# Optimization experiments

Hardware: AMD Instinct MI355X
Metric: run time of the kernel (lower is better)

The kernel has to match this reference:

```python
import jax, jax.numpy as jnp
import numpy as np
import math

N_HEAD = 16
DEG = 2
EPS = 1e-7


def setup_inputs() -> dict:
    key = jax.random.key(0)
    k1, k2 = jax.random.split(key)
    B, T, C = 2, 2048, 1024
    x = jax.random.normal(k1, (B, T, C), dtype=jnp.float32)
    W = jax.random.normal(k2, (3 * C + N_HEAD, C), dtype=jnp.float32) * (1.0 / math.sqrt(C))
    return {"x": x, "W": W}


def reference(x, W):
    # JacobAttentionLayer.forward with attention_kernel='powerref' (AttentionReference,
    # deg=2, scale=1/sqrt(hs), eps=1e-7, log-space power softmax, gating=True).
    B, T, C = x.shape
    nh = N_HEAD
    hs = C // nh
    scale = 1.0 / math.sqrt(hs)

    qkvgr = jnp.einsum('btc,oc->bto', x, W)  # [B,T,3C+nh]
    q, k, v = (qkvgr[..., :C], qkvgr[..., C:2 * C], qkvgr[..., 2 * C:3 * C])
    log_g = jax.nn.log_sigmoid(qkvgr[..., 3 * C:].astype(jnp.float32))  # [B,T,nh]
    log_G = jnp.cumsum(log_g, axis=1).transpose(0, 2, 1)  # [B,nh,T]

    def heads(a):  # [B,T,C] -> [B,nh,T,hs]
        return a.reshape(B, T, nh, hs).transpose(0, 2, 1, 3)

    Q, K, V = heads(q), heads(k), heads(v)

    S = jnp.einsum('bhtd,bhsd->bhts', Q, K)  # [B,nh,T,T]
    # log-space power attention: deg*log(|S|+eps) + log(scale) + gating
    Tm = DEG * jnp.log(jnp.abs(S) + EPS) + jnp.log(jnp.float32(scale))
    Z = Tm + log_G[..., :, None] - log_G[..., None, :]
    mask = jnp.tril(jnp.ones((T, T), dtype=bool))
    Z = jnp.where(mask, Z, -jnp.inf)
    Z_rowmax = jax.lax.stop_gradient(jnp.max(Z, axis=-1, keepdims=True))
    P = jnp.exp(Z - Z_rowmax)  # deg even -> no sign correction

    norm = jnp.sum(P, axis=-1)  # [B,nh,T]
    O = jnp.einsum('bhts,bhsd->bhtd', P, V)
    y = O / norm[..., None]
    return y.transpose(0, 2, 1, 3).reshape(B, T, C)
```

## Files before the change

### kernel.cpp

```cpp
#include <hip/hip_runtime.h>
#include <math.h>

typedef __attribute__((ext_vector_type(4))) float f32x4;
typedef __attribute__((ext_vector_type(8))) short short8;

__device__ __forceinline__ unsigned short f2bf(float f) {
    union { float f; unsigned u; } v; v.f = f;
    unsigned r = v.u + 0x7FFFu + ((v.u >> 16) & 1u);
    return (unsigned short)(r >> 16);
}
__device__ __forceinline__ unsigned short f2bf_trunc(float f) {
    union { float f; unsigned u; } v; v.f = f;
    return (unsigned short)(v.u >> 16);
}
__device__ __forceinline__ float bf2f(unsigned short h) {
    union { unsigned u; float f; } v; v.u = ((unsigned)h) << 16;
    return v.f;
}

__device__ __forceinline__ f32x4 mfma_bf16(short8 a, short8 b, f32x4 c) {
    return __builtin_amdgcn_mfma_f32_16x16x32_bf16(a, b, c, 0, 0, 0);
}

__device__ __forceinline__ void gload_lds16(const unsigned short* g, unsigned short* l) {
    __builtin_amdgcn_global_load_lds(
        (const __attribute__((address_space(1))) void*)g,
        (__attribute__((address_space(3))) void*)l, 16, 0, 0);
}

__global__ void split_all(const float* __restrict__ x,
                          unsigned short* __restrict__ xh, unsigned short* __restrict__ xl,
                          const float* __restrict__ Wm,
                          unsigned short* __restrict__ wh, unsigned short* __restrict__ wl,
                          int nx4, int nw4)
{
    int i = blockIdx.x * 256 + threadIdx.x;
    const float* src; unsigned short* dh; unsigned short* dl; int j;
    if (i < nx4) { src = x; dh = xh; dl = xl; j = i; }
    else if (i < nx4 + nw4) { src = Wm; dh = wh; dl = wl; j = i - nx4; }
    else return;
    float4 v = ((const float4*)src)[j];
    ushort4 h, l;
    h.x = f2bf(v.x); l.x = f2bf(v.x - bf2f(h.x));
    h.y = f2bf(v.y); l.y = f2bf(v.y - bf2f(h.y));
    h.z = f2bf(v.z); l.z = f2bf(v.z - bf2f(h.z));
    h.w = f2bf(v.w); l.w = f2bf(v.w - bf2f(h.w));
    ((ushort4*)dh)[j] = h;
    ((ushort4*)dl)[j] = l;
}

__global__ __launch_bounds__(256, 2)
void gemm_proj(const unsigned short* __restrict__ xh, const unsigned short* __restrict__ xl,
               const unsigned short* __restrict__ wh, const unsigned short* __restrict__ wl,
               unsigned short* __restrict__ Qh, unsigned short* __restrict__ Ql,
               unsigned short* __restrict__ Kh, unsigned short* __restrict__ Kl,
               unsigned short* __restrict__ Vtg, float* __restrict__ gbuf)
{
    __shared__ __align__(16) unsigned short Ah[2][128][32];
    __shared__ __align__(16) unsigned short Al[2][128][32];
    __shared__ __align__(16) unsigned short Bh[2][128][32];
    __shared__ __align__(16) unsigned short Bl[2][128][32];

    const int mt = blockIdx.x & 31;
    const int nt = blockIdx.x >> 5;
    const int m0 = mt * 128, n0 = nt * 128;
    const int tid = threadIdx.x;
    const int w = tid >> 6, l = tid & 63;
    const int wm = w >> 1, wn = w & 1;
    const int lr = l & 15, lq = l >> 4;
    const int xs = (lr >> 1) & 3;
    const bool needLo = (nt < 16) || (nt == 24);

    f32x4 acc[4][4];
#pragma unroll
    for (int i = 0; i < 4; ++i)
#pragma unroll
        for (int j = 0; j < 4; ++j) acc[i][j] = (f32x4){0.f, 0.f, 0.f, 0.f};

    const int srow = tid >> 2;
    const int sp = tid & 3;

    auto STAGE = [&](int bsel, int k0) {
#pragma unroll
        for (int p = 0; p < 2; ++p) {
            int r = srow + p * 64;
            int sc = (sp ^ ((r >> 1) & 3)) * 8;
            int o = n0 + r;
            int oc = o < 3088 ? o : 3087;
            gload_lds16(&xh[(size_t)(m0 + r) * 1024 + k0 + sc], &Ah[bsel][r][sp * 8]);
            gload_lds16(&wh[(size_t)oc * 1024 + k0 + sc],       &Bh[bsel][r][sp * 8]);
            if (needLo) {
                gload_lds16(&xl[(size_t)(m0 + r) * 1024 + k0 + sc], &Al[bsel][r][sp * 8]);
                gload_lds16(&wl[(size_t)oc * 1024 + k0 + sc],       &Bl[bsel][r][sp * 8]);
            }
        }
    };

    STAGE(0, 0);
    __asm__ volatile("s_waitcnt vmcnt(0)" ::: "memory");
    __syncthreads();

    int cur = 0;
    for (int k0 = 0; k0 < 1024; k0 += 32) {
        if (k0 + 32 < 1024) STAGE(cur ^ 1, k0 + 32);

        short8 ah[4], bh4[4], al4[4], bl4[4];
#pragma unroll
        for (int i = 0; i < 4; ++i) {
            ah[i]  = *(const short8*)&Ah[cur][wm * 64 + i * 16 + lr][(lq ^ xs) * 8];
            bh4[i] = *(const short8*)&Bh[cur][wn * 64 + i * 16 + lr][(lq ^ xs) * 8];
        }
        if (needLo) {
#pragma unroll
            for (int i = 0; i < 4; ++i) {
                al4[i] = *(const short8*)&Al[cur][wm * 64 + i * 16 + lr][(lq ^ xs) * 8];
                bl4[i] = *(const short8*)&Bl[cur][wn * 64 + i * 16 + lr][(lq ^ xs) * 8];
            }
        }
#pragma unroll
        for (int i = 0; i < 4; ++i)
#pragma unroll
            for (int j = 0; j < 4; ++j) {
                acc[i][j] = mfma_bf16(ah[i], bh4[j], acc[i][j]);
                if (needLo) {
                    acc[i][j] = mfma_bf16(ah[i], bl4[j], acc[i][j]);
                    acc[i][j] = mfma_bf16(al4[i], bh4[j], acc[i][j]);
                }
            }

        __asm__ volatile("s_waitcnt vmcnt(0)" ::: "memory");
        __syncthreads();
        cur ^= 1;
    }

#pragma unroll
    for (int i = 0; i < 4; ++i) {
        int nrow0 = m0 + wm * 64 + i * 16 + lq * 4;
        int b = nrow0 >> 11;
        int tbase = nrow0 & 2047;
#pragma unroll
        for (int j = 0; j < 4; ++j) {
            int o = n0 + wn * 64 + j * 16 + lr;
            if (o < 1024) {
                int h = o >> 6, d = o & 63;
                size_t base = ((size_t)(b * 16 + h) * 2048 + tbase) * 64 + d;
#pragma unroll
                for (int r = 0; r < 4; ++r) {
                    float v = acc[i][j][r];
                    unsigned short hi_ = f2bf(v);
                    unsigned short lo_ = f2bf(v - bf2f(hi_));
                    Qh[base + (size_t)r * 64] = hi_;
                    Ql[base + (size_t)r * 64] = lo_;
                }
            } else if (o < 2048) {
                int oo = o - 1024;
                int h = oo >> 6, d = oo & 63;
                size_t base = ((size_t)(b * 16 + h) * 2048 + tbase) * 64 + d;
#pragma unroll
                for (int r = 0; r < 4; ++r) {
                    float v = acc[i][j][r];
                    unsigned short hi_ = f2bf(v);
                    unsigned short lo_ = f2bf(v - bf2f(hi_));
                    Kh[base + (size_t)r * 64] = hi_;
                    Kl[base + (size_t)r * 64] = lo_;
                }
            } else if (o < 3072) {
                int oo = o - 2048;
                int h = oo >> 6, d = oo & 63;
                size_t base = ((size_t)(b * 16 + h) * 64 + d) * 2048 + tbase;
                ushort4 pk;
                pk.x = f2bf(acc[i][j][0]);
                pk.y = f2bf(acc[i][j][1]);
                pk.z = f2bf(acc[i][j][2]);
                pk.w = f2bf(acc[i][j][3]);
                *(ushort4*)&Vtg[base] = pk;
            } else if (o < 3088) {
                int og = o - 3072;
#pragma unroll
                for (int r = 0; r < 4; ++r)
                    gbuf[(size_t)(nrow0 + r) * 16 + og] = acc[i][j][r];
            }
        }
    }
}

__global__ void gate_scan(const float* __restrict__ g, float* __restrict__ lg)
{
    const int bh = blockIdx.x;
    const int b = bh >> 4, h = bh & 15;
    const int tid = threadIdx.x;
    __shared__ float part[256];

    float vals[8];
    float run = 0.f;
#pragma unroll
    for (int j = 0; j < 8; ++j) {
        int t = tid * 8 + j;
        float x = g[(size_t)(b * 2048 + t) * 16 + h];
        float ls = fminf(x, 0.f) - log1pf(__expf(-fabsf(x)));
        run += ls * 1.4426950408889634f;
        vals[j] = run;
    }
    part[tid] = run;
    __syncthreads();
    for (int ofs = 1; ofs < 256; ofs <<= 1) {
        float add = (tid >= ofs) ? part[tid - ofs] : 0.f;
        __syncthreads();
        part[tid] += add;
        __syncthreads();
    }
    float excl = part[tid] - run;
#pragma unroll
    for (int j = 0; j < 8; ++j)
        lg[(size_t)bh * 2048 + tid * 8 + j] = excl + vals[j];
}

__global__ __launch_bounds__(256, 3)
void attn_fwd(const unsigned short* __restrict__ Qh, const unsigned short* __restrict__ Ql,
              const unsigned short* __restrict__ Kh, const unsigned short* __restrict__ Kl,
              const unsigned short* __restrict__ Vtg, const float* __restrict__ lg,
              float* __restrict__ out)
{
    __shared__ __align__(16) unsigned short kh[2][64][64];
    __shared__ __align__(16) unsigned short kl[2][64][64];
    __shared__ __align__(16) unsigned short pl[4][16][64];

    const int bid = blockIdx.x;
    const int x8 = bid & 7;
    const int k  = bid >> 3;
    const int bh = x8 + 8 * (k & 3);
    const int m  = k >> 2;
    const int qi = 31 - m;
    const int tid = threadIdx.x;
    const int w = tid >> 6, l = tid & 63;
    const int lr = l & 15, lq = l >> 4;
    const int xk = lr & 7;
    const int q0 = qi * 64;
    const int myrow0 = q0 + w * 16;

    const size_t qoff = ((size_t)bh * 2048 + myrow0 + lr) * 64;
    short8 qh8[2], ql8[2];
    qh8[0] = *(const short8*)&Qh[qoff + lq * 8];
    qh8[1] = *(const short8*)&Qh[qoff + 32 + lq * 8];
    ql8[0] = *(const short8*)&Ql[qoff + lq * 8];
    ql8[1] = *(const short8*)&Ql[qoff + 32 + lq * 8];

    float gq2[4];
#pragma unroll
    for (int r = 0; r < 4; ++r)
        gq2[r] = lg[(size_t)bh * 2048 + myrow0 + lq * 4 + r] - 3.0f;

    f32x4 ls4 = (f32x4){0.f, 0.f, 0.f, 0.f};
    f32x4 o4[4];
#pragma unroll
    for (int i = 0; i < 4; ++i) o4[i] = (f32x4){0.f, 0.f, 0.f, 0.f};

    short8 ones8;
#pragma unroll
    for (int j = 0; j < 8; ++j) ones8[j] = (short)0x3F80;

    const int srow = tid >> 3;
    const int schunk = tid & 7;

    const unsigned short* Kh_b = Kh + (size_t)bh * 2048 * 64;
    const unsigned short* Kl_b = Kl + (size_t)bh * 2048 * 64;
    const unsigned short* Vt_b = Vtg + (size_t)bh * 64 * 2048;

    auto STAGE = [&](int bsel, int kv0) {
#pragma unroll
        for (int p = 0; p < 2; ++p) {
            int r = srow + p * 32;
            int sc = (schunk ^ (r & 7)) * 8;
            gload_lds16(&Kh_b[(size_t)(kv0 + r) * 64 + sc], &kh[bsel][r][schunk * 8]);
            gload_lds16(&Kl_b[(size_t)(kv0 + r) * 64 + sc], &kl[bsel][r][schunk * 8]);
        }
    };

    STAGE(0, 0);
    __asm__ volatile("s_waitcnt vmcnt(0)" ::: "memory");
    __syncthreads();

    int cur = 0;
    for (int kv0 = 0; kv0 <= q0; kv0 += 64) {
        uint4 vreg[8];
#pragma unroll
        for (int ds_ = 0; ds_ < 4; ++ds_) {
            const unsigned short* vp = &Vt_b[(size_t)(ds_ * 16 + lr) * 2048 + kv0 + lq * 8];
            vreg[ds_ * 2]     = *(const uint4*)vp;
            vreg[ds_ * 2 + 1] = *(const uint4*)(vp + 32);
        }
        if (kv0 + 64 <= q0) STAGE(cur ^ 1, kv0 + 64);

        float gsl[4];
#pragma unroll
        for (int js = 0; js < 4; ++js)
            gsl[js] = lg[(size_t)bh * 2048 + kv0 + js * 16 + lr];

        f32x4 sa[4];
#pragma unroll
        for (int js = 0; js < 4; ++js) sa[js] = (f32x4){0.f, 0.f, 0.f, 0.f};
#pragma unroll
        for (int js = 0; js < 4; ++js)
#pragma unroll
            for (int ks = 0; ks < 2; ++ks) {
                short8 kb  = *(const short8*)&kh[cur][js * 16 + lr][((ks * 4 + lq) ^ xk) << 3];
                short8 kbl = *(const short8*)&kl[cur][js * 16 + lr][((ks * 4 + lq) ^ xk) << 3];
                sa[js] = mfma_bf16(qh8[ks], kb,  sa[js]);
                sa[js] = mfma_bf16(qh8[ks], kbl, sa[js]);
                sa[js] = mfma_bf16(ql8[ks], kb,  sa[js]);
            }

        const bool diag = (kv0 == q0);
#pragma unroll
        for (int js = 0; js < 4; ++js) {
            float ga = gsl[js];
#pragma unroll
            for (int r = 0; r < 4; ++r) {
                float a = fabsf(sa[js][r]) + 1e-7f;
                float ex = exp2f(gq2[r] - ga);
                float wv = a * a * ex;
                if (diag && (js * 16 + lr > w * 16 + lq * 4 + r)) wv = 0.f;
                sa[js][r] = wv;
            }
        }

#pragma unroll
        for (int js = 0; js < 4; ++js)
#pragma unroll
            for (int r = 0; r < 4; ++r) {
                int prow = lq * 4 + r;
                int cch = (js * 2 + (lr >> 3)) ^ (prow & 7);
                pl[w][prow][(cch << 3) | (lr & 7)] = f2bf_trunc(sa[js][r]);
            }
        __asm__ volatile("s_waitcnt lgkmcnt(0)" ::: "memory");
        __builtin_amdgcn_sched_barrier(0);

        short8 pa0 = *(const short8*)&pl[w][lr][((0 + lq) ^ xk) << 3];
        short8 pa1 = *(const short8*)&pl[w][lr][((4 + lq) ^ xk) << 3];

        ls4 = mfma_bf16(pa0, ones8, ls4);
        ls4 = mfma_bf16(pa1, ones8, ls4);
#pragma unroll
        for (int ds_ = 0; ds_ < 4; ++ds_) {
            short8 vb0 = *(const short8*)&vreg[ds_ * 2];
            short8 vb1 = *(const short8*)&vreg[ds_ * 2 + 1];
            o4[ds_] = mfma_bf16(pa0, vb0, o4[ds_]);
            o4[ds_] = mfma_bf16(pa1, vb1, o4[ds_]);
        }

        __asm__ volatile("s_waitcnt vmcnt(0)" ::: "memory");
        __syncthreads();
        cur ^= 1;
    }

    const int b = bh >> 4, h = bh & 15;
#pragma unroll
    for (int ds_ = 0; ds_ < 4; ++ds_)
#pragma unroll
        for (int r = 0; r < 4; ++r) {
            int t = myrow0 + lq * 4 + r;
            out[(size_t)(b * 2048 + t) * 1024 + h * 64 + ds_ * 16 + lr] =
                o4[ds_][r] / ls4[r];
        }
}

extern "C" void kernel_launch(void* const* d_in, const int* in_sizes, int n_in,
                              void* d_out, int out_size, void* d_ws, size_t ws_size,
                              hipStream_t stream)
{
    const float* x = (const float*)d_in[0];
    const float* W = (const float*)d_in[1];
    float* out = (float*)d_out;

    const size_t NX = 4194304;
    const size_t NW = 3162112;
    const size_t NQ = 4194304;

    char* ws = (char*)d_ws;
    size_t off = 0;
    auto alloc = [&](size_t bytes) -> void* {
        void* p = ws + off;
        off += (bytes + 255) & ~(size_t)255;
        return p;
    };
    unsigned short* xh = (unsigned short*)alloc(NX * 2);
    unsigned short* xl = (unsigned short*)alloc(NX * 2);
    unsigned short* wh = (unsigned short*)alloc(NW * 2);
    unsigned short* wl = (unsigned short*)alloc(NW * 2);
    unsigned short* Qh = (unsigned short*)alloc(NQ * 2);
    unsigned short* Ql = (unsigned short*)alloc(NQ * 2);
    unsigned short* Kh = (unsigned short*)alloc(NQ * 2);
    unsigned short* Kl = (unsigned short*)alloc(NQ * 2);
    unsigned short* Vt = (unsigned short*)alloc(NQ * 2);
    float* g  = (float*)alloc(65536 * 4);
    float* lg = (float*)alloc(65536 * 4);
    if (off > ws_size) return;

    const int nx4 = (int)(NX / 4), nw4 = (int)(NW / 4);
    split_all<<<(nx4 + nw4 + 255) / 256, 256, 0, stream>>>(x, xh, xl, W, wh, wl, nx4, nw4);
    gemm_proj<<<800, 256, 0, stream>>>(xh, xl, wh, wl, Qh, Ql, Kh, Kl, Vt, g);
    gate_scan<<<32, 256, 0, stream>>>(g, lg);
    attn_fwd<<<1024, 256, 0, stream>>>(Qh, Ql, Kh, Kl, Vt, lg, out);
}
```

Baseline: 183.7 us.

## Drop LDS staging in projection GEMM, load MFMA operands directly from global

The projection GEMM no longer double-buffers A/B tiles through shared memory. Each wave now reads its bf16 hi/lo operand fragments straight from global memory (relying on L1/L2 for reuse), which removes the barriers and LDS traffic. Launch bounds are raised to 3 blocks per SM to gain occupancy. The cost is that operands shared across waves are fetched redundantly from cache and there is no explicit prefetch overlap, so load latency may become exposed.

```diff
diff --git a/kernel.cpp b/kernel.cpp
--- a/kernel.cpp
+++ b/kernel.cpp
@@ -49,18 +49,13 @@
     ((ushort4*)dl)[j] = l;
 }
 
-__global__ __launch_bounds__(256, 2)
+__global__ __launch_bounds__(256, 3)
 void gemm_proj(const unsigned short* __restrict__ xh, const unsigned short* __restrict__ xl,
                const unsigned short* __restrict__ wh, const unsigned short* __restrict__ wl,
                unsigned short* __restrict__ Qh, unsigned short* __restrict__ Ql,
                unsigned short* __restrict__ Kh, unsigned short* __restrict__ Kl,
                unsigned short* __restrict__ Vtg, float* __restrict__ gbuf)
 {
-    __shared__ __align__(16) unsigned short Ah[2][128][32];
-    __shared__ __align__(16) unsigned short Al[2][128][32];
-    __shared__ __align__(16) unsigned short Bh[2][128][32];
-    __shared__ __align__(16) unsigned short Bl[2][128][32];
-
     const int mt = blockIdx.x & 31;
     const int nt = blockIdx.x >> 5;
     const int m0 = mt * 128, n0 = nt * 128;
@@ -68,7 +63,6 @@
     const int w = tid >> 6, l = tid & 63;
     const int wm = w >> 1, wn = w & 1;
     const int lr = l & 15, lq = l >> 4;
-    const int xs = (lr >> 1) & 3;
     const bool needLo = (nt < 16) || (nt == 24);
 
     f32x4 acc[4][4];
@@ -77,45 +71,34 @@
 #pragma unroll
         for (int j = 0; j < 4; ++j) acc[i][j] = (f32x4){0.f, 0.f, 0.f, 0.f};
 
-    const int srow = tid >> 2;
-    const int sp = tid & 3;
-
-    auto STAGE = [&](int bsel, int k0) {
-#pragma unroll
-        for (int p = 0; p < 2; ++p) {
-            int r = srow + p * 64;
-            int sc = (sp ^ ((r >> 1) & 3)) * 8;
-            int o = n0 + r;
-            int oc = o < 3088 ? o : 3087;
-            gload_lds16(&xh[(size_t)(m0 + r) * 1024 + k0 + sc], &Ah[bsel][r][sp * 8]);
-            gload_lds16(&wh[(size_t)oc * 1024 + k0 + sc],       &Bh[bsel][r][sp * 8]);
-            if (needLo) {
-                gload_lds16(&xl[(size_t)(m0 + r) * 1024 + k0 + sc], &Al[bsel][r][sp * 8]);
-                gload_lds16(&wl[(size_t)oc * 1024 + k0 + sc],       &Bl[bsel][r][sp * 8]);
-            }
-        }
-    };
-
-    STAGE(0, 0);
-    __asm__ volatile("s_waitcnt vmcnt(0)" ::: "memory");
-    __syncthreads();
-
-    int cur = 0;
+    const size_t aoff = (size_t)(m0 + wm * 64 + lr) * 1024 + lq * 8;
+    const unsigned short* xA  = xh + aoff;
+    const unsigned short* xAl = xl + aoff;
+    const unsigned short* wB[4];
+    const unsigned short* wBl[4];
+#pragma unroll
+    for (int j = 0; j < 4; ++j) {
+        int o = n0 + wn * 64 + j * 16 + lr;
+        int oc = o < 3088 ? o : 3087;
+        wB[j]  = wh + (size_t)oc * 1024 + lq * 8;
+        wBl[j] = wl + (size_t)oc * 1024 + lq * 8;
+    }
+
     for (int k0 = 0; k0 < 1024; k0 += 32) {
-        if (k0 + 32 < 1024) STAGE(cur ^ 1, k0 + 32);
-
         short8 ah[4], bh4[4], al4[4], bl4[4];
 #pragma unroll
-        for (int i = 0; i < 4; ++i) {
-            ah[i]  = *(const short8*)&Ah[cur][wm * 64 + i * 16 + lr][(lq ^ xs) * 8];
-            bh4[i] = *(const short8*)&Bh[cur][wn * 64 + i * 16 + lr][(lq ^ xs) * 8];
-        }
+        for (int i = 0; i < 4; ++i)
+            ah[i]  = *(const short8*)(xA + (size_t)i * 16 * 1024 + k0);
+#pragma unroll
+        for (int j = 0; j < 4; ++j)
+            bh4[j] = *(const short8*)(wB[j] + k0);
         if (needLo) {
 #pragma unroll
-            for (int i = 0; i < 4; ++i) {
-                al4[i] = *(const short8*)&Al[cur][wm * 64 + i * 16 + lr][(lq ^ xs) * 8];
-                bl4[i] = *(const short8*)&Bl[cur][wn * 64 + i * 16 + lr][(lq ^ xs) * 8];
-            }
+            for (int i = 0; i < 4; ++i)
+                al4[i] = *(const short8*)(xAl + (size_t)i * 16 * 1024 + k0);
+#pragma unroll
+            for (int j = 0; j < 4; ++j)
+                bl4[j] = *(const short8*)(wBl[j] + k0);
         }
 #pragma unroll
         for (int i = 0; i < 4; ++i)
@@ -127,10 +110,6 @@
                     acc[i][j] = mfma_bf16(al4[i], bh4[j], acc[i][j]);
                 }
             }
-
-        __asm__ volatile("s_waitcnt vmcnt(0)" ::: "memory");
-        __syncthreads();
-        cur ^= 1;
     }
 
 #pragma unroll
```

Measured after the change: 287.4 us. 1.56x slower.

## Single-buffer lo-part tiles in projection GEMM and raise occupancy to three blocks

Applied to the files above, without the earlier changes.

The projection GEMM now keeps the bf16 low-part A/B tiles in a single buffer that is loaded inside the current k-step instead of double-buffering them. The hi-part MFMAs run first while the lo loads are in flight, followed by a partial vmcnt wait and a barrier. The freed LDS and a launch-bounds change target three resident blocks per CU. Block order is also remapped so the heavier tile column (nt=24, which needs the lo correction) is scheduled first. In exchange, the lo loads are less hidden, each step gets an extra barrier, and the tighter register budget could cause spills.

```diff
diff --git a/kernel.cpp b/kernel.cpp
--- a/kernel.cpp
+++ b/kernel.cpp
@@ -49,7 +49,7 @@
     ((ushort4*)dl)[j] = l;
 }
 
-__global__ __launch_bounds__(256, 2)
+__global__ __launch_bounds__(256, 3)
 void gemm_proj(const unsigned short* __restrict__ xh, const unsigned short* __restrict__ xl,
                const unsigned short* __restrict__ wh, const unsigned short* __restrict__ wl,
                unsigned short* __restrict__ Qh, unsigned short* __restrict__ Ql,
@@ -57,12 +57,13 @@
                unsigned short* __restrict__ Vtg, float* __restrict__ gbuf)
 {
     __shared__ __align__(16) unsigned short Ah[2][128][32];
-    __shared__ __align__(16) unsigned short Al[2][128][32];
     __shared__ __align__(16) unsigned short Bh[2][128][32];
-    __shared__ __align__(16) unsigned short Bl[2][128][32];
+    __shared__ __align__(16) unsigned short Al[128][32];
+    __shared__ __align__(16) unsigned short Bl[128][32];
 
     const int mt = blockIdx.x & 31;
-    const int nt = blockIdx.x >> 5;
+    const int ntr = blockIdx.x >> 5;
+    const int nt = (ntr == 0) ? 24 : ntr - 1;
     const int m0 = mt * 128, n0 = nt * 128;
     const int tid = threadIdx.x;
     const int w = tid >> 6, l = tid & 63;
@@ -80,7 +81,7 @@
     const int srow = tid >> 2;
     const int sp = tid & 3;
 
-    auto STAGE = [&](int bsel, int k0) {
+    auto STAGE_HI = [&](int bsel, int k0) {
 #pragma unroll
         for (int p = 0; p < 2; ++p) {
             int r = srow + p * 64;
@@ -89,44 +90,64 @@
             int oc = o < 3088 ? o : 3087;
             gload_lds16(&xh[(size_t)(m0 + r) * 1024 + k0 + sc], &Ah[bsel][r][sp * 8]);
             gload_lds16(&wh[(size_t)oc * 1024 + k0 + sc],       &Bh[bsel][r][sp * 8]);
-            if (needLo) {
-                gload_lds16(&xl[(size_t)(m0 + r) * 1024 + k0 + sc], &Al[bsel][r][sp * 8]);
-                gload_lds16(&wl[(size_t)oc * 1024 + k0 + sc],       &Bl[bsel][r][sp * 8]);
-            }
         }
     };
-
-    STAGE(0, 0);
+    auto STAGE_LO = [&](int k0) {
+#pragma unroll
+        for (int p = 0; p < 2; ++p) {
+            int r = srow + p * 64;
+            int sc = (sp ^ ((r >> 1) & 3)) * 8;
+            int o = n0 + r;
+            int oc = o < 3088 ? o : 3087;
+            gload_lds16(&xl[(size_t)(m0 + r) * 1024 + k0 + sc], &Al[r][sp * 8]);
+            gload_lds16(&wl[(size_t)oc * 1024 + k0 + sc],       &Bl[r][sp * 8]);
+        }
+    };
+
+    STAGE_HI(0, 0);
     __asm__ volatile("s_waitcnt vmcnt(0)" ::: "memory");
     __syncthreads();
 
     int cur = 0;
-    for (int k0 = 0; k0 < 1024; k0 += 32) {
-        if (k0 + 32 < 1024) STAGE(cur ^ 1, k0 + 32);
-
-        short8 ah[4], bh4[4], al4[4], bl4[4];
+    for (int t = 0; t < 32; ++t) {
+        const int k0 = t * 32;
+        if (needLo) STAGE_LO(k0);
+        if (t + 1 < 32) STAGE_HI(cur ^ 1, k0 + 32);
+
+        short8 ah[4], bh4[4];
 #pragma unroll
         for (int i = 0; i < 4; ++i) {
             ah[i]  = *(const short8*)&Ah[cur][wm * 64 + i * 16 + lr][(lq ^ xs) * 8];
             bh4[i] = *(const short8*)&Bh[cur][wn * 64 + i * 16 + lr][(lq ^ xs) * 8];
         }
+#pragma unroll
+        for (int i = 0; i < 4; ++i)
+#pragma unroll
+            for (int j = 0; j < 4; ++j)
+                acc[i][j] = mfma_bf16(ah[i], bh4[j], acc[i][j]);
+
         if (needLo) {
+            if (t + 1 < 32) {
+                __asm__ volatile("s_waitcnt vmcnt(4)" ::: "memory");
+            } else {
+                __asm__ volatile("s_waitcnt vmcnt(0)" ::: "memory");
+            }
+            __syncthreads();
+
+            short8 al4[4], bl4[4];
 #pragma unroll
             for (int i = 0; i < 4; ++i) {
-                al4[i] = *(const short8*)&Al[cur][wm * 64 + i * 16 + lr][(lq ^ xs) * 8];
-                bl4[i] = *(const short8*)&Bl[cur][wn * 64 + i * 16 + lr][(lq ^ xs) * 8];
-            }
-        }
-#pragma unroll
-        for (int i = 0; i < 4; ++i)
-#pragma unroll
-            for (int j = 0; j < 4; ++j) {
-                acc[i][j] = mfma_bf16(ah[i], bh4[j], acc[i][j]);
-                if (needLo) {
+                al4[i] = *(const short8*)&Al[wm * 64 + i * 16 + lr][(lq ^ xs) * 8];
+                bl4[i] = *(const short8*)&Bl[wn * 64 + i * 16 + lr][(lq ^ xs) * 8];
+            }
+#pragma unroll
+            for (int i = 0; i < 4; ++i)
+#pragma unroll
+                for (int j = 0; j < 4; ++j) {
                     acc[i][j] = mfma_bf16(ah[i], bl4[j], acc[i][j]);
                     acc[i][j] = mfma_bf16(al4[i], bh4[j], acc[i][j]);
                 }
-            }
+        }
 
         __asm__ volatile("s_waitcnt vmcnt(0)" ::: "memory");
         __syncthreads();
```

Result: no change. 181.2 us (-1.4%).
